# Kernel optimization log

Measured on AMD Instinct MI355X. Metric: run time of the kernel, lower is better.

The kernel has to match this reference:

```python
import jax, jax.numpy as jnp
import numpy as np

N_NODES = 50000

def gcn_conv(x, src, dst, W, b, n_nodes):
    # PyG GCNConv: add self-loops, symmetric deg^{-1/2} normalization,
    # linear transform, scatter-add aggregation (source -> target), bias.
    loop = jnp.arange(n_nodes, dtype=src.dtype)
    src2 = jnp.concatenate([src, loop])
    dst2 = jnp.concatenate([dst, loop])
    deg = jax.ops.segment_sum(jnp.ones_like(dst2, dtype=x.dtype), dst2, num_segments=n_nodes)
    dinv = jnp.where(deg > 0, jax.lax.rsqrt(deg), 0.0)
    norm = dinv[src2] * dinv[dst2]  # [E + N]
    h = x @ W                        # [N, out]
    msg = h[src2] * norm[:, None]    # gather + scale
    out = jax.ops.segment_sum(msg, dst2, num_segments=n_nodes)
    return out + b

def setup_inputs() -> dict:
    key = jax.random.key(0)
    k1, k2, k3, k4 = jax.random.split(key, 4)
    x = jax.random.normal(k1, (N_NODES, 64), dtype=jnp.float32)
    edge_index = jax.random.randint(k2, (2, 800000), 0, N_NODES, dtype=jnp.int64)
    # Glorot-ish init for weights
    W1 = jax.random.normal(k3, (64, 128), dtype=jnp.float32) * (1.0 / np.sqrt(64))
    b1 = jnp.zeros((128,), dtype=jnp.float32)
    W2 = jax.random.normal(k4, (128, 8), dtype=jnp.float32) * (1.0 / np.sqrt(128))
    b2 = jnp.zeros((8,), dtype=jnp.float32)
    return {"x": x, "edge_index": edge_index, "W1": W1, "b1": b1, "W2": W2, "b2": b2}

def reference(x, edge_index, W1, b1, W2, b2):
    src, dst = edge_index[0], edge_index[1]
    h = gcn_conv(x, src, dst, W1, b1, N_NODES)
    h = jax.nn.relu(h)
    out = gcn_conv(h, src, dst, W2, b2, N_NODES)
    return out
```

## Files before the change

kernel.cpp:

```cpp
#include <hip/hip_runtime.h>

#define IN1 64
#define MID 128
#define OUT2 8
#define YPAD 136
#define TPAD 68
#define CAP 64

__device__ __forceinline__ unsigned short f2bf(float f) {
    unsigned int u = __float_as_uint(f);
    unsigned int r = (u + 0x7fff + ((u >> 16) & 1)) >> 16;
    return (unsigned short)r;
}
__device__ __forceinline__ float bflo(unsigned int u) { return __uint_as_float(u << 16); }
__device__ __forceinline__ float bfhi(unsigned int u) { return __uint_as_float(u & 0xffff0000u); }

__global__ __launch_bounds__(256) void k_fillp(const int* __restrict__ src,
                                               const int* __restrict__ dst,
                                               int* __restrict__ cnt,
                                               unsigned short* __restrict__ col,
                                               int E4, int E, int npx, int slices) {
    int xcd = blockIdx.x & 7;
    int slice = blockIdx.x >> 3;
    int lo = xcd * npx, hi = lo + npx;
    int eps = (E4 + slices - 1) / slices;
    int g0 = slice * eps, g1 = min(E4, g0 + eps);
    int g = g0 + (int)threadIdx.x;
    if (g < g1) {
        int4 dv = ((const int4*)dst)[g];
        for (;;) {
            int gn = g + 256;
            bool has = gn < g1;
            int4 dn;
            if (has) dn = ((const int4*)dst)[gn];
            if (dv.x >= lo && dv.x < hi) {
                int p = atomicAdd(&cnt[dv.x], 1);
                if (p < CAP) col[dv.x * CAP + p] = (unsigned short)src[4 * g];
            }
            if (dv.y >= lo && dv.y < hi) {
                int p = atomicAdd(&cnt[dv.y], 1);
                if (p < CAP) col[dv.y * CAP + p] = (unsigned short)src[4 * g + 1];
            }
            if (dv.z >= lo && dv.z < hi) {
                int p = atomicAdd(&cnt[dv.z], 1);
                if (p < CAP) col[dv.z * CAP + p] = (unsigned short)src[4 * g + 2];
            }
            if (dv.w >= lo && dv.w < hi) {
                int p = atomicAdd(&cnt[dv.w], 1);
                if (p < CAP) col[dv.w * CAP + p] = (unsigned short)src[4 * g + 3];
            }
            if (!has) break;
            dv = dn;
            g = gn;
        }
    }
    if (blockIdx.x == 0 && threadIdx.x == 0) {
        for (int e = E4 * 4; e < E; ++e) {
            int d = dst[e];
            int p = atomicAdd(&cnt[d], 1);
            if (p < CAP) col[d * CAP + p] = (unsigned short)src[e];
        }
    }
}

__global__ void k_prescale(const float4* __restrict__ x4, const int* __restrict__ cnt,
                           float* __restrict__ dinv, ushort4* __restrict__ xb4, int n16) {
    int gid = blockIdx.x * blockDim.x + threadIdx.x;
    if (gid >= n16) return;
    int row = gid >> 4;
    float d = rsqrtf((float)(cnt[row] + 1));
    if ((gid & 15) == 0) dinv[row] = d;
    float4 vx = x4[gid];
    ushort4 p;
    p.x = f2bf(vx.x * d); p.y = f2bf(vx.y * d);
    p.z = f2bf(vx.z * d); p.w = f2bf(vx.w * d);
    xb4[gid] = p;
}

__global__ __launch_bounds__(256) void k_node(const uint4* __restrict__ xb4,
                                              const int* __restrict__ cnt,
                                              const unsigned short* __restrict__ col,
                                              const float* __restrict__ dinv,
                                              const float* __restrict__ W1,
                                              const float* __restrict__ b1,
                                              const float* __restrict__ W2,
                                              float* __restrict__ z, int n) {
    __shared__ float w2s[MID * OUT2];
    __shared__ float tS[4][8][TPAD];
    __shared__ float yS[4][8][YPAD];

    int t = threadIdx.x;
    ((float4*)w2s)[t] = ((const float4*)W2)[t];

    int lane = t & 63, wave = t >> 6;
    int g = lane >> 3;
    int fl = lane & 7;
    int row0 = blockIdx.x * 32 + wave * 8;
    int row = row0 + g;
    bool valid = row < n;

    float a0=0.f,a1=0.f,a2=0.f,a3=0.f,a4=0.f,a5=0.f,a6=0.f,a7=0.f;
    int deg = 0, base = 0;
    if (valid) {
        deg = min(cnt[row], CAP);
        base = row * CAP;
        uint4 u = xb4[(size_t)row * 8 + fl];
        a0 = bflo(u.x); a1 = bfhi(u.x); a2 = bflo(u.y); a3 = bfhi(u.y);
        a4 = bflo(u.z); a5 = bfhi(u.z); a6 = bflo(u.w); a7 = bfhi(u.w);
    }
    int cv = (deg >= 8) ? col[base + fl] : 0;
    int j = 0;
    for (; j + 8 <= deg; j += 8) {
        int cvn = (j + 16 <= deg) ? col[base + j + 8 + fl] : 0;
#pragma unroll
        for (int p = 0; p < 8; ++p) {
            int s = __shfl(cv, (g << 3) + p, 64);
            uint4 u = xb4[(size_t)s * 8 + fl];
            a0 += bflo(u.x); a1 += bfhi(u.x); a2 += bflo(u.y); a3 += bfhi(u.y);
            a4 += bflo(u.z); a5 += bfhi(u.z); a6 += bflo(u.w); a7 += bfhi(u.w);
        }
        cv = cvn;
    }
    int rem = deg - j;
    if (rem > 0) {
        int cvr = col[base + min(j + fl, CAP - 1)];
#pragma unroll
        for (int p = 0; p < 8; ++p) {
            if (p < rem) {
                int s = __shfl(cvr, (g << 3) + p, 64);
                uint4 u = xb4[(size_t)s * 8 + fl];
                a0 += bflo(u.x); a1 += bfhi(u.x); a2 += bflo(u.y); a3 += bfhi(u.y);
                a4 += bflo(u.z); a5 += bfhi(u.z); a6 += bflo(u.w); a7 += bfhi(u.w);
            }
        }
    }
    {
        float4 w0 = {a0, a1, a2, a3};
        float4 w1v = {a4, a5, a6, a7};
        *(float4*)&tS[wave][g][8 * fl] = w0;
        *(float4*)&tS[wave][g][8 * fl + 4] = w1v;
    }

    float dnd[8];
#pragma unroll
    for (int k = 0; k < 8; ++k) dnd[k] = dinv[min(row0 + k, n - 1)];

    float ya[8], yb[8];
#pragma unroll
    for (int i = 0; i < 8; ++i) { ya[i] = 0.f; yb[i] = 0.f; }
#pragma unroll 2
    for (int k4 = 0; k4 < IN1; k4 += 4) {
        float4 tv[8];
#pragma unroll
        for (int nd = 0; nd < 8; ++nd) tv[nd] = *(const float4*)&tS[wave][nd][k4];
#pragma unroll
        for (int kk = 0; kk < 4; ++kk) {
            int k = k4 + kk;
            float wa = W1[k * MID + lane];
            float wb = W1[k * MID + lane + 64];
#pragma unroll
            for (int nd = 0; nd < 8; ++nd) {
                float e = (&tv[nd].x)[kk];
                ya[nd] = fmaf(e, wa, ya[nd]);
                yb[nd] = fmaf(e, wb, yb[nd]);
            }
        }
    }
    float bl = b1[lane], bh = b1[lane + 64];
#pragma unroll
    for (int nd = 0; nd < 8; ++nd) {
        yS[wave][nd][lane] = fmaxf(fmaf(ya[nd], dnd[nd], bl), 0.f);
        yS[wave][nd][lane + 64] = fmaxf(fmaf(yb[nd], dnd[nd], bh), 0.f);
    }

    __syncthreads();

    int nd2 = lane >> 3, ch = lane & 7;
    float p[OUT2];
#pragma unroll
    for (int c = 0; c < OUT2; ++c) p[c] = 0.0f;
#pragma unroll
    for (int kk = 0; kk < 16; ++kk) {
        int k = kk * 8 + ch;
        float yk = yS[wave][nd2][k];
        float4 wlo = *(const float4*)&w2s[k * OUT2];
        float4 whi = *(const float4*)&w2s[k * OUT2 + 4];
        p[0] = fmaf(yk, wlo.x, p[0]); p[1] = fmaf(yk, wlo.y, p[1]);
        p[2] = fmaf(yk, wlo.z, p[2]); p[3] = fmaf(yk, wlo.w, p[3]);
        p[4] = fmaf(yk, whi.x, p[4]); p[5] = fmaf(yk, whi.y, p[5]);
        p[6] = fmaf(yk, whi.z, p[6]); p[7] = fmaf(yk, whi.w, p[7]);
    }
#pragma unroll
    for (int off = 1; off < 8; off <<= 1) {
#pragma unroll
        for (int c = 0; c < OUT2; ++c) p[c] += __shfl_xor(p[c], off, 64);
    }
    int rw = row0 + nd2;
    if (rw < n) {
        z[(size_t)rw * OUT2 + ch] = p[ch] * dinv[rw];
    }
}

__global__ __launch_bounds__(256) void k_gather2(const int* __restrict__ cnt,
                                                 const unsigned short* __restrict__ col,
                                                 const float* __restrict__ z,
                                                 const float* __restrict__ dinv,
                                                 const float* __restrict__ b2,
                                                 float* __restrict__ out, int n) {
    int t = threadIdx.x, lane = t & 63, wave = t >> 6;
    int node = blockIdx.x * 4 + wave;
    if (node >= n) return;
    int nb = lane >> 3, c = lane & 7;
    float acc = (nb == 0) ? z[(size_t)node * OUT2 + c] : 0.0f;
    int deg = min(cnt[node], CAP);
    int base = node * CAP;
    int j = nb;
    if (j + 8 < deg) {
        int s0 = col[base + j], s1 = col[base + j + 8];
        for (; j + 8 < deg;) {
            int jn = j + 16;
            int t0 = 0, t1 = 0;
            bool has = jn + 8 < deg;
            if (has) { t0 = col[base + jn]; t1 = col[base + jn + 8]; }
            acc += z[(size_t)s0 * OUT2 + c] + z[(size_t)s1 * OUT2 + c];
            j = jn;
            if (!has) break;
            s0 = t0; s1 = t1;
        }
    }
    if (j < deg) acc += z[(size_t)col[base + j] * OUT2 + c];
#pragma unroll
    for (int off = 8; off < 64; off <<= 1) acc += __shfl_xor(acc, off, 64);
    if (lane < OUT2) out[(size_t)node * OUT2 + lane] = fmaf(acc, dinv[node], b2[lane]);
}

extern "C" void kernel_launch(void* const* d_in, const int* in_sizes, int n_in,
                              void* d_out, int out_size, void* d_ws, size_t ws_size,
                              hipStream_t stream) {
    const float* x  = (const float*)d_in[0];
    const int*   ei = (const int*)d_in[1];
    const float* W1 = (const float*)d_in[2];
    const float* b1 = (const float*)d_in[3];
    const float* W2 = (const float*)d_in[4];
    const float* b2 = (const float*)d_in[5];
    float* out = (float*)d_out;

    int N = in_sizes[0] / IN1;
    int E = in_sizes[1] / 2;
    const int* src = ei;
    const int* dst = ei + E;

    int* cnt = (int*)d_ws;
    unsigned short* col = (unsigned short*)(cnt + N);
    float* dinv = (float*)(col + (size_t)N * CAP);
    float* z = dinv + N;
    unsigned short* xb = (unsigned short*)(z + (size_t)N * OUT2);

    const int B = 256;
    int E4 = E / 4;
    int npx = (N + 7) / 8;
    int slices = 256;

    hipMemsetAsync(cnt, 0, (size_t)N * sizeof(int), stream);
    k_fillp<<<slices * 8, B, 0, stream>>>(src, dst, cnt, col, E4, E, npx, slices);
    k_prescale<<<((size_t)N * 16 + B - 1) / B, B, 0, stream>>>((const float4*)x, cnt, dinv,
                                                               (ushort4*)xb, N * 16);
    k_node<<<(N + 31) / 32, 256, 0, stream>>>((const uint4*)xb, cnt, col, dinv, W1, b1, W2, z, N);
    k_gather2<<<(N + 3) / 4, 256, 0, stream>>>(cnt, col, z, dinv, b2, out, N);
}
```

Before: 162.1 us.

## Fuse pipeline into two cooperative kernels with grid-wide syncs

```diff
diff --git a/kernel.cpp b/kernel.cpp
--- a/kernel.cpp
+++ b/kernel.cpp
@@ -1,4 +1,7 @@
 #include <hip/hip_runtime.h>
+#include <hip/hip_cooperative_groups.h>
+
+namespace cg = cooperative_groups;
 
 #define IN1 64
 #define MID 128
@@ -15,11 +18,14 @@
 __device__ __forceinline__ float bflo(unsigned int u) { return __uint_as_float(u << 16); }
 __device__ __forceinline__ float bfhi(unsigned int u) { return __uint_as_float(u & 0xffff0000u); }
 
-__global__ __launch_bounds__(256) void k_fillp(const int* __restrict__ src,
-                                               const int* __restrict__ dst,
-                                               int* __restrict__ cnt,
-                                               unsigned short* __restrict__ col,
-                                               int E4, int E, int npx, int slices) {
+__global__ __launch_bounds__(256, 8) void k_fill(const int* __restrict__ src,
+                                                 const int* __restrict__ dst,
+                                                 int* __restrict__ cnt,
+                                                 unsigned short* __restrict__ col,
+                                                 int E4, int E, int npx, int slices, int N) {
+    for (int i = blockIdx.x * 256 + (int)threadIdx.x; i < N; i += gridDim.x * 256) cnt[i] = 0;
+    cg::this_grid().sync();
+
     int xcd = blockIdx.x & 7;
     int slice = blockIdx.x >> 3;
     int lo = xcd * npx, hi = lo + npx;
@@ -63,175 +69,178 @@
     }
 }
 
-__global__ void k_prescale(const float4* __restrict__ x4, const int* __restrict__ cnt,
-                           float* __restrict__ dinv, ushort4* __restrict__ xb4, int n16) {
-    int gid = blockIdx.x * blockDim.x + threadIdx.x;
-    if (gid >= n16) return;
-    int row = gid >> 4;
-    float d = rsqrtf((float)(cnt[row] + 1));
-    if ((gid & 15) == 0) dinv[row] = d;
-    float4 vx = x4[gid];
-    ushort4 p;
-    p.x = f2bf(vx.x * d); p.y = f2bf(vx.y * d);
-    p.z = f2bf(vx.z * d); p.w = f2bf(vx.w * d);
-    xb4[gid] = p;
-}
-
-__global__ __launch_bounds__(256) void k_node(const uint4* __restrict__ xb4,
-                                              const int* __restrict__ cnt,
-                                              const unsigned short* __restrict__ col,
-                                              const float* __restrict__ dinv,
-                                              const float* __restrict__ W1,
-                                              const float* __restrict__ b1,
-                                              const float* __restrict__ W2,
-                                              float* __restrict__ z, int n) {
+__global__ __launch_bounds__(256, 4) void k_mlp(const float4* __restrict__ x4,
+                                                const int* __restrict__ cnt,
+                                                const unsigned short* __restrict__ col,
+                                                float* dinv,
+                                                unsigned short* xb,
+                                                const float* __restrict__ W1,
+                                                const float* __restrict__ b1,
+                                                const float* __restrict__ W2,
+                                                const float* __restrict__ b2,
+                                                float* z,
+                                                float* __restrict__ out,
+                                                int n, int n16) {
     __shared__ float w2s[MID * OUT2];
     __shared__ float tS[4][8][TPAD];
     __shared__ float yS[4][8][YPAD];
 
     int t = threadIdx.x;
+
+    for (int gid = blockIdx.x * 256 + t; gid < n16; gid += gridDim.x * 256) {
+        int row = gid >> 4;
+        float d = rsqrtf((float)(cnt[row] + 1));
+        if ((gid & 15) == 0) dinv[row] = d;
+        float4 vx = x4[gid];
+        ushort4 pv;
+        pv.x = f2bf(vx.x * d); pv.y = f2bf(vx.y * d);
+        pv.z = f2bf(vx.z * d); pv.w = f2bf(vx.w * d);
+        ((ushort4*)xb)[gid] = pv;
+    }
+    cg::this_grid().sync();
+
     ((float4*)w2s)[t] = ((const float4*)W2)[t];
+    __syncthreads();
 
     int lane = t & 63, wave = t >> 6;
     int g = lane >> 3;
     int fl = lane & 7;
-    int row0 = blockIdx.x * 32 + wave * 8;
-    int row = row0 + g;
-    bool valid = row < n;
-
-    float a0=0.f,a1=0.f,a2=0.f,a3=0.f,a4=0.f,a5=0.f,a6=0.f,a7=0.f;
-    int deg = 0, base = 0;
-    if (valid) {
-        deg = min(cnt[row], CAP);
-        base = row * CAP;
-        uint4 u = xb4[(size_t)row * 8 + fl];
-        a0 = bflo(u.x); a1 = bfhi(u.x); a2 = bflo(u.y); a3 = bfhi(u.y);
-        a4 = bflo(u.z); a5 = bfhi(u.z); a6 = bflo(u.w); a7 = bfhi(u.w);
-    }
-    int cv = (deg >= 8) ? col[base + fl] : 0;
-    int j = 0;
-    for (; j + 8 <= deg; j += 8) {
-        int cvn = (j + 16 <= deg) ? col[base + j + 8 + fl] : 0;
-#pragma unroll
-        for (int p = 0; p < 8; ++p) {
-            int s = __shfl(cv, (g << 3) + p, 64);
-            uint4 u = xb4[(size_t)s * 8 + fl];
-            a0 += bflo(u.x); a1 += bfhi(u.x); a2 += bflo(u.y); a3 += bfhi(u.y);
-            a4 += bflo(u.z); a5 += bfhi(u.z); a6 += bflo(u.w); a7 += bfhi(u.w);
-        }
-        cv = cvn;
-    }
-    int rem = deg - j;
-    if (rem > 0) {
-        int cvr = col[base + min(j + fl, CAP - 1)];
-#pragma unroll
-        for (int p = 0; p < 8; ++p) {
-            if (p < rem) {
-                int s = __shfl(cvr, (g << 3) + p, 64);
+    const uint4* xb4 = (const uint4*)xb;
+
+    int nlb = (n + 31) >> 5;
+    for (int lb = blockIdx.x; lb < nlb; lb += gridDim.x) {
+        int row0 = lb * 32 + wave * 8;
+        int row = row0 + g;
+        bool valid = row < n;
+
+        float a0=0.f,a1=0.f,a2=0.f,a3=0.f,a4=0.f,a5=0.f,a6=0.f,a7=0.f;
+        int deg = 0, base = 0;
+        if (valid) {
+            deg = min(cnt[row], CAP);
+            base = row * CAP;
+            uint4 u = xb4[(size_t)row * 8 + fl];
+            a0 = bflo(u.x); a1 = bfhi(u.x); a2 = bflo(u.y); a3 = bfhi(u.y);
+            a4 = bflo(u.z); a5 = bfhi(u.z); a6 = bflo(u.w); a7 = bfhi(u.w);
+        }
+        int cv = (deg >= 8) ? col[base + fl] : 0;
+        int j = 0;
+        for (; j + 8 <= deg; j += 8) {
+            int cvn = (j + 16 <= deg) ? col[base + j + 8 + fl] : 0;
+#pragma unroll
+            for (int p = 0; p < 8; ++p) {
+                int s = __shfl(cv, (g << 3) + p, 64);
                 uint4 u = xb4[(size_t)s * 8 + fl];
                 a0 += bflo(u.x); a1 += bfhi(u.x); a2 += bflo(u.y); a3 += bfhi(u.y);
                 a4 += bflo(u.z); a5 += bfhi(u.z); a6 += bflo(u.w); a7 += bfhi(u.w);
             }
-        }
-    }
+            cv = cvn;
+        }
+        int rem = deg - j;
+        if (rem > 0) {
+            int cvr = col[base + min(j + fl, CAP - 1)];
+#pragma unroll
+            for (int p = 0; p < 8; ++p) {
+                if (p < rem) {
+                    int s = __shfl(cvr, (g << 3) + p, 64);
+                    uint4 u = xb4[(size_t)s * 8 + fl];
+                    a0 += bflo(u.x); a1 += bfhi(u.x); a2 += bflo(u.y); a3 += bfhi(u.y);
+                    a4 += bflo(u.z); a5 += bfhi(u.z); a6 += bflo(u.w); a7 += bfhi(u.w);
+                }
+            }
+        }
+        {
+            float4 w0 = {a0, a1, a2, a3};
+            float4 w1v = {a4, a5, a6, a7};
+            *(float4*)&tS[wave][g][8 * fl] = w0;
+            *(float4*)&tS[wave][g][8 * fl + 4] = w1v;
+        }
+
+        float dnd[8];
+#pragma unroll
+        for (int k = 0; k < 8; ++k) dnd[k] = dinv[min(row0 + k, n - 1)];
+
+        float ya[8], yb[8];
+#pragma unroll
+        for (int i = 0; i < 8; ++i) { ya[i] = 0.f; yb[i] = 0.f; }
+#pragma unroll 2
+        for (int k4 = 0; k4 < IN1; k4 += 4) {
+            float4 tv[8];
+#pragma unroll
+            for (int nd = 0; nd < 8; ++nd) tv[nd] = *(const float4*)&tS[wave][nd][k4];
+#pragma unroll
+            for (int kk = 0; kk < 4; ++kk) {
+                int k = k4 + kk;
+                float wa = W1[k * MID + lane];
+                float wb = W1[k * MID + lane + 64];
+#pragma unroll
+                for (int nd = 0; nd < 8; ++nd) {
+                    float e = (&tv[nd].x)[kk];
+                    ya[nd] = fmaf(e, wa, ya[nd]);
+                    yb[nd] = fmaf(e, wb, yb[nd]);
+                }
+            }
+        }
+        float bl = b1[lane], bh = b1[lane + 64];
+#pragma unroll
+        for (int nd = 0; nd < 8; ++nd) {
+            yS[wave][nd][lane] = fmaxf(fmaf(ya[nd], dnd[nd], bl), 0.f);
+            yS[wave][nd][lane + 64] = fmaxf(fmaf(yb[nd], dnd[nd], bh), 0.f);
+        }
+
+        int nd2 = lane >> 3, ch = lane & 7;
+        float p[OUT2];
+#pragma unroll
+        for (int c = 0; c < OUT2; ++c) p[c] = 0.0f;
+#pragma unroll
+        for (int kk = 0; kk < 16; ++kk) {
+            int k = kk * 8 + ch;
+            float yk = yS[wave][nd2][k];
+            float4 wlo = *(const float4*)&w2s[k * OUT2];
+            float4 whi = *(const float4*)&w2s[k * OUT2 + 4];
+            p[0] = fmaf(yk, wlo.x, p[0]); p[1] = fmaf(yk, wlo.y, p[1]);
+            p[2] = fmaf(yk, wlo.z, p[2]); p[3] = fmaf(yk, wlo.w, p[3]);
+            p[4] = fmaf(yk, whi.x, p[4]); p[5] = fmaf(yk, whi.y, p[5]);
+            p[6] = fmaf(yk, whi.z, p[6]); p[7] = fmaf(yk, whi.w, p[7]);
+        }
+#pragma unroll
+        for (int off = 1; off < 8; off <<= 1) {
+#pragma unroll
+            for (int c = 0; c < OUT2; ++c) p[c] += __shfl_xor(p[c], off, 64);
+        }
+        int rw = row0 + nd2;
+        if (rw < n) {
+            z[(size_t)rw * OUT2 + ch] = p[ch] * dinv[rw];
+        }
+    }
+
+    cg::this_grid().sync();
+
     {
-        float4 w0 = {a0, a1, a2, a3};
-        float4 w1v = {a4, a5, a6, a7};
-        *(float4*)&tS[wave][g][8 * fl] = w0;
-        *(float4*)&tS[wave][g][8 * fl + 4] = w1v;
-    }
-
-    float dnd[8];
-#pragma unroll
-    for (int k = 0; k < 8; ++k) dnd[k] = dinv[min(row0 + k, n - 1)];
-
-    float ya[8], yb[8];
-#pragma unroll
-    for (int i = 0; i < 8; ++i) { ya[i] = 0.f; yb[i] = 0.f; }
-#pragma unroll 2
-    for (int k4 = 0; k4 < IN1; k4 += 4) {
-        float4 tv[8];
-#pragma unroll
-        for (int nd = 0; nd < 8; ++nd) tv[nd] = *(const float4*)&tS[wave][nd][k4];
-#pragma unroll
-        for (int kk = 0; kk < 4; ++kk) {
-            int k = k4 + kk;
-            float wa = W1[k * MID + lane];
-            float wb = W1[k * MID + lane + 64];
-#pragma unroll
-            for (int nd = 0; nd < 8; ++nd) {
-                float e = (&tv[nd].x)[kk];
-                ya[nd] = fmaf(e, wa, ya[nd]);
-                yb[nd] = fmaf(e, wb, yb[nd]);
-            }
-        }
-    }
-    float bl = b1[lane], bh = b1[lane + 64];
-#pragma unroll
-    for (int nd = 0; nd < 8; ++nd) {
-        yS[wave][nd][lane] = fmaxf(fmaf(ya[nd], dnd[nd], bl), 0.f);
-        yS[wave][nd][lane + 64] = fmaxf(fmaf(yb[nd], dnd[nd], bh), 0.f);
-    }
-
-    __syncthreads();
-
-    int nd2 = lane >> 3, ch = lane & 7;
-    float p[OUT2];
-#pragma unroll
-    for (int c = 0; c < OUT2; ++c) p[c] = 0.0f;
-#pragma unroll
-    for (int kk = 0; kk < 16; ++kk) {
-        int k = kk * 8 + ch;
-        float yk = yS[wave][nd2][k];
-        float4 wlo = *(const float4*)&w2s[k * OUT2];
-        float4 whi = *(const float4*)&w2s[k * OUT2 + 4];
-        p[0] = fmaf(yk, wlo.x, p[0]); p[1] = fmaf(yk, wlo.y, p[1]);
-        p[2] = fmaf(yk, wlo.z, p[2]); p[3] = fmaf(yk, wlo.w, p[3]);
-        p[4] = fmaf(yk, whi.x, p[4]); p[5] = fmaf(yk, whi.y, p[5]);
-        p[6] = fmaf(yk, whi.z, p[6]); p[7] = fmaf(yk, whi.w, p[7]);
-    }
-#pragma unroll
-    for (int off = 1; off < 8; off <<= 1) {
-#pragma unroll
-        for (int c = 0; c < OUT2; ++c) p[c] += __shfl_xor(p[c], off, 64);
-    }
-    int rw = row0 + nd2;
-    if (rw < n) {
-        z[(size_t)rw * OUT2 + ch] = p[ch] * dinv[rw];
-    }
-}
-
-__global__ __launch_bounds__(256) void k_gather2(const int* __restrict__ cnt,
-                                                 const unsigned short* __restrict__ col,
-                                                 const float* __restrict__ z,
-                                                 const float* __restrict__ dinv,
-                                                 const float* __restrict__ b2,
-                                                 float* __restrict__ out, int n) {
-    int t = threadIdx.x, lane = t & 63, wave = t >> 6;
-    int node = blockIdx.x * 4 + wave;
-    if (node >= n) return;
-    int nb = lane >> 3, c = lane & 7;
-    float acc = (nb == 0) ? z[(size_t)node * OUT2 + c] : 0.0f;
-    int deg = min(cnt[node], CAP);
-    int base = node * CAP;
-    int j = nb;
-    if (j + 8 < deg) {
-        int s0 = col[base + j], s1 = col[base + j + 8];
-        for (; j + 8 < deg;) {
-            int jn = j + 16;
-            int t0 = 0, t1 = 0;
-            bool has = jn + 8 < deg;
-            if (has) { t0 = col[base + jn]; t1 = col[base + jn + 8]; }
-            acc += z[(size_t)s0 * OUT2 + c] + z[(size_t)s1 * OUT2 + c];
-            j = jn;
-            if (!has) break;
-            s0 = t0; s1 = t1;
-        }
-    }
-    if (j < deg) acc += z[(size_t)col[base + j] * OUT2 + c];
-#pragma unroll
-    for (int off = 8; off < 64; off <<= 1) acc += __shfl_xor(acc, off, 64);
-    if (lane < OUT2) out[(size_t)node * OUT2 + lane] = fmaf(acc, dinv[node], b2[lane]);
+        int nb = lane >> 3, c = lane & 7;
+        for (int node = blockIdx.x * 4 + wave; node < n; node += gridDim.x * 4) {
+            float acc = (nb == 0) ? z[(size_t)node * OUT2 + c] : 0.0f;
+            int deg = min(cnt[node], CAP);
+            int base = node * CAP;
+            int j = nb;
+            if (j + 8 < deg) {
+                int s0 = col[base + j], s1 = col[base + j + 8];
+                for (; j + 8 < deg;) {
+                    int jn = j + 16;
+                    int t0 = 0, t1 = 0;
+                    bool has = jn + 8 < deg;
+                    if (has) { t0 = col[base + jn]; t1 = col[base + jn + 8]; }
+                    acc += z[(size_t)s0 * OUT2 + c] + z[(size_t)s1 * OUT2 + c];
+                    j = jn;
+                    if (!has) break;
+                    s0 = t0; s1 = t1;
+                }
+            }
+            if (j < deg) acc += z[(size_t)col[base + j] * OUT2 + c];
+#pragma unroll
+            for (int off = 8; off < 64; off <<= 1) acc += __shfl_xor(acc, off, 64);
+            if (lane < OUT2) out[(size_t)node * OUT2 + lane] = fmaf(acc, dinv[node], b2[lane]);
+        }
+    }
 }
 
 extern "C" void kernel_launch(void* const* d_in, const int* in_sizes, int n_in,
@@ -256,15 +265,37 @@
     float* z = dinv + N;
     unsigned short* xb = (unsigned short*)(z + (size_t)N * OUT2);
 
-    const int B = 256;
     int E4 = E / 4;
     int npx = (N + 7) / 8;
+    int n16 = N * 16;
+    const float4* x4 = (const float4*)x;
+
+    static int occ1 = 0, occ2 = 0;
+    if (occ1 == 0) {
+        int a = 0, b = 0;
+        hipError_t ea = hipOccupancyMaxActiveBlocksPerMultiprocessor(&a, (const void*)k_fill, 256, 0);
+        hipError_t eb = hipOccupancyMaxActiveBlocksPerMultiprocessor(&b, (const void*)k_mlp, 256, 0);
+        occ1 = (ea == hipSuccess && a > 0) ? a : 8;
+        occ2 = (eb == hipSuccess && b > 0) ? b : 4;
+        (void)hipGetLastError();
+    }
     int slices = 256;
-
-    hipMemsetAsync(cnt, 0, (size_t)N * sizeof(int), stream);
-    k_fillp<<<slices * 8, B, 0, stream>>>(src, dst, cnt, col, E4, E, npx, slices);
-    k_prescale<<<((size_t)N * 16 + B - 1) / B, B, 0, stream>>>((const float4*)x, cnt, dinv,
-                                                               (ushort4*)xb, N * 16);
-    k_node<<<(N + 31) / 32, 256, 0, stream>>>((const uint4*)xb, cnt, col, dinv, W1, b1, W2, z, N);
-    k_gather2<<<(N + 3) / 4, 256, 0, stream>>>(cnt, col, z, dinv, b2, out, N);
+    if (slices * 8 > occ1 * 256) slices = (occ1 * 256) / 8;
+    if (slices < 1) slices = 1;
+    int grid1 = slices * 8;
+    int grid2 = 1024;
+    if (grid2 > occ2 * 256) grid2 = occ2 * 256;
+    if (grid2 < 1) grid2 = 1;
+
+    {
+        void* args[] = {(void*)&src, (void*)&dst, (void*)&cnt, (void*)&col,
+                        (void*)&E4, (void*)&E, (void*)&npx, (void*)&slices, (void*)&N};
+        hipLaunchCooperativeKernel((const void*)k_fill, dim3(grid1), dim3(256), args, 0, stream);
+    }
+    {
+        void* args[] = {(void*)&x4, (void*)&cnt, (void*)&col, (void*)&dinv, (void*)&xb,
+                        (void*)&W1, (void*)&b1, (void*)&W2, (void*)&b2,
+                        (void*)&z, (void*)&out, (void*)&N, (void*)&n16};
+        hipLaunchCooperativeKernel((const void*)k_mlp, dim3(grid2), dim3(256), args, 0, stream);
+    }
 }
```

New measurement: 460.4 us. 2.84x slower.

## Fold prescale into fill kernel and compute degree normalization on the fly

Applied to the files above, without the earlier changes.

```diff
diff --git a/kernel.cpp b/kernel.cpp
--- a/kernel.cpp
+++ b/kernel.cpp
@@ -15,11 +15,21 @@
 __device__ __forceinline__ float bflo(unsigned int u) { return __uint_as_float(u << 16); }
 __device__ __forceinline__ float bfhi(unsigned int u) { return __uint_as_float(u & 0xffff0000u); }
 
-__global__ __launch_bounds__(256) void k_fillp(const int* __restrict__ src,
-                                               const int* __restrict__ dst,
-                                               int* __restrict__ cnt,
-                                               unsigned short* __restrict__ col,
-                                               int E4, int E, int npx, int slices) {
+__global__ __launch_bounds__(256) void k_fill(const int* __restrict__ src,
+                                              const int* __restrict__ dst,
+                                              int* __restrict__ cnt,
+                                              unsigned short* __restrict__ col,
+                                              const float4* __restrict__ x4,
+                                              ushort4* __restrict__ xb4,
+                                              int E4, int E, int npx, int slices, int n16) {
+    for (int gid = blockIdx.x * 256 + (int)threadIdx.x; gid < n16; gid += gridDim.x * 256) {
+        float4 vx = x4[gid];
+        ushort4 pv;
+        pv.x = f2bf(vx.x); pv.y = f2bf(vx.y);
+        pv.z = f2bf(vx.z); pv.w = f2bf(vx.w);
+        xb4[gid] = pv;
+    }
+
     int xcd = blockIdx.x & 7;
     int slice = blockIdx.x >> 3;
     int lo = xcd * npx, hi = lo + npx;
@@ -28,29 +38,30 @@
     int g = g0 + (int)threadIdx.x;
     if (g < g1) {
         int4 dv = ((const int4*)dst)[g];
+        int4 sv = ((const int4*)src)[g];
         for (;;) {
             int gn = g + 256;
             bool has = gn < g1;
-            int4 dn;
-            if (has) dn = ((const int4*)dst)[gn];
+            int4 dn, sn;
+            if (has) { dn = ((const int4*)dst)[gn]; sn = ((const int4*)src)[gn]; }
             if (dv.x >= lo && dv.x < hi) {
                 int p = atomicAdd(&cnt[dv.x], 1);
-                if (p < CAP) col[dv.x * CAP + p] = (unsigned short)src[4 * g];
+                if (p < CAP) col[dv.x * CAP + p] = (unsigned short)sv.x;
             }
             if (dv.y >= lo && dv.y < hi) {
                 int p = atomicAdd(&cnt[dv.y], 1);
-                if (p < CAP) col[dv.y * CAP + p] = (unsigned short)src[4 * g + 1];
+                if (p < CAP) col[dv.y * CAP + p] = (unsigned short)sv.y;
             }
             if (dv.z >= lo && dv.z < hi) {
                 int p = atomicAdd(&cnt[dv.z], 1);
-                if (p < CAP) col[dv.z * CAP + p] = (unsigned short)src[4 * g + 2];
+                if (p < CAP) col[dv.z * CAP + p] = (unsigned short)sv.z;
             }
             if (dv.w >= lo && dv.w < hi) {
                 int p = atomicAdd(&cnt[dv.w], 1);
-                if (p < CAP) col[dv.w * CAP + p] = (unsigned short)src[4 * g + 3];
+                if (p < CAP) col[dv.w * CAP + p] = (unsigned short)sv.w;
             }
             if (!has) break;
-            dv = dn;
+            dv = dn; sv = sn;
             g = gn;
         }
     }
@@ -63,24 +74,9 @@
     }
 }
 
-__global__ void k_prescale(const float4* __restrict__ x4, const int* __restrict__ cnt,
-                           float* __restrict__ dinv, ushort4* __restrict__ xb4, int n16) {
-    int gid = blockIdx.x * blockDim.x + threadIdx.x;
-    if (gid >= n16) return;
-    int row = gid >> 4;
-    float d = rsqrtf((float)(cnt[row] + 1));
-    if ((gid & 15) == 0) dinv[row] = d;
-    float4 vx = x4[gid];
-    ushort4 p;
-    p.x = f2bf(vx.x * d); p.y = f2bf(vx.y * d);
-    p.z = f2bf(vx.z * d); p.w = f2bf(vx.w * d);
-    xb4[gid] = p;
-}
-
 __global__ __launch_bounds__(256) void k_node(const uint4* __restrict__ xb4,
                                               const int* __restrict__ cnt,
                                               const unsigned short* __restrict__ col,
-                                              const float* __restrict__ dinv,
                                               const float* __restrict__ W1,
                                               const float* __restrict__ b1,
                                               const float* __restrict__ W2,
@@ -102,11 +98,15 @@
     float a0=0.f,a1=0.f,a2=0.f,a3=0.f,a4=0.f,a5=0.f,a6=0.f,a7=0.f;
     int deg = 0, base = 0;
     if (valid) {
-        deg = min(cnt[row], CAP);
+        int c0 = cnt[row];
+        deg = min(c0, CAP);
         base = row * CAP;
+        float dself = rsqrtf((float)(c0 + 1));
         uint4 u = xb4[(size_t)row * 8 + fl];
-        a0 = bflo(u.x); a1 = bfhi(u.x); a2 = bflo(u.y); a3 = bfhi(u.y);
-        a4 = bflo(u.z); a5 = bfhi(u.z); a6 = bflo(u.w); a7 = bfhi(u.w);
+        a0 = dself * bflo(u.x); a1 = dself * bfhi(u.x);
+        a2 = dself * bflo(u.y); a3 = dself * bfhi(u.y);
+        a4 = dself * bflo(u.z); a5 = dself * bfhi(u.z);
+        a6 = dself * bflo(u.w); a7 = dself * bfhi(u.w);
     }
     int cv = (deg >= 8) ? col[base + fl] : 0;
     int j = 0;
@@ -115,9 +115,13 @@
 #pragma unroll
         for (int p = 0; p < 8; ++p) {
             int s = __shfl(cv, (g << 3) + p, 64);
+            int cs = cnt[s];
             uint4 u = xb4[(size_t)s * 8 + fl];
-            a0 += bflo(u.x); a1 += bfhi(u.x); a2 += bflo(u.y); a3 += bfhi(u.y);
-            a4 += bflo(u.z); a5 += bfhi(u.z); a6 += bflo(u.w); a7 += bfhi(u.w);
+            float ds = rsqrtf((float)(cs + 1));
+            a0 = fmaf(ds, bflo(u.x), a0); a1 = fmaf(ds, bfhi(u.x), a1);
+            a2 = fmaf(ds, bflo(u.y), a2); a3 = fmaf(ds, bfhi(u.y), a3);
+            a4 = fmaf(ds, bflo(u.z), a4); a5 = fmaf(ds, bfhi(u.z), a5);
+            a6 = fmaf(ds, bflo(u.w), a6); a7 = fmaf(ds, bfhi(u.w), a7);
         }
         cv = cvn;
     }
@@ -128,9 +132,13 @@
         for (int p = 0; p < 8; ++p) {
             if (p < rem) {
                 int s = __shfl(cvr, (g << 3) + p, 64);
+                int cs = cnt[s];
                 uint4 u = xb4[(size_t)s * 8 + fl];
-                a0 += bflo(u.x); a1 += bfhi(u.x); a2 += bflo(u.y); a3 += bfhi(u.y);
-                a4 += bflo(u.z); a5 += bfhi(u.z); a6 += bflo(u.w); a7 += bfhi(u.w);
+                float ds = rsqrtf((float)(cs + 1));
+                a0 = fmaf(ds, bflo(u.x), a0); a1 = fmaf(ds, bfhi(u.x), a1);
+                a2 = fmaf(ds, bflo(u.y), a2); a3 = fmaf(ds, bfhi(u.y), a3);
+                a4 = fmaf(ds, bflo(u.z), a4); a5 = fmaf(ds, bfhi(u.z), a5);
+                a6 = fmaf(ds, bflo(u.w), a6); a7 = fmaf(ds, bfhi(u.w), a7);
             }
         }
     }
@@ -143,7 +151,10 @@
 
     float dnd[8];
 #pragma unroll
-    for (int k = 0; k < 8; ++k) dnd[k] = dinv[min(row0 + k, n - 1)];
+    for (int k = 0; k < 8; ++k) {
+        int ck = cnt[min(row0 + k, n - 1)];
+        dnd[k] = rsqrtf((float)(ck + 1));
+    }
 
     float ya[8], yb[8];
 #pragma unroll
@@ -197,14 +208,13 @@
     }
     int rw = row0 + nd2;
     if (rw < n) {
-        z[(size_t)rw * OUT2 + ch] = p[ch] * dinv[rw];
+        z[(size_t)rw * OUT2 + ch] = p[ch] * dnd[nd2];
     }
 }
 
 __global__ __launch_bounds__(256) void k_gather2(const int* __restrict__ cnt,
                                                  const unsigned short* __restrict__ col,
                                                  const float* __restrict__ z,
-                                                 const float* __restrict__ dinv,
                                                  const float* __restrict__ b2,
                                                  float* __restrict__ out, int n) {
     int t = threadIdx.x, lane = t & 63, wave = t >> 6;
@@ -212,7 +222,8 @@
     if (node >= n) return;
     int nb = lane >> 3, c = lane & 7;
     float acc = (nb == 0) ? z[(size_t)node * OUT2 + c] : 0.0f;
-    int deg = min(cnt[node], CAP);
+    int c0 = cnt[node];
+    int deg = min(c0, CAP);
     int base = node * CAP;
     int j = nb;
     if (j + 8 < deg) {
@@ -231,7 +242,7 @@
     if (j < deg) acc += z[(size_t)col[base + j] * OUT2 + c];
 #pragma unroll
     for (int off = 8; off < 64; off <<= 1) acc += __shfl_xor(acc, off, 64);
-    if (lane < OUT2) out[(size_t)node * OUT2 + lane] = fmaf(acc, dinv[node], b2[lane]);
+    if (lane < OUT2) out[(size_t)node * OUT2 + lane] = fmaf(acc, rsqrtf((float)(c0 + 1)), b2[lane]);
 }
 
 extern "C" void kernel_launch(void* const* d_in, const int* in_sizes, int n_in,
@@ -252,19 +263,19 @@
 
     int* cnt = (int*)d_ws;
     unsigned short* col = (unsigned short*)(cnt + N);
-    float* dinv = (float*)(col + (size_t)N * CAP);
-    float* z = dinv + N;
+    float* z = (float*)(col + (size_t)N * CAP);
     unsigned short* xb = (unsigned short*)(z + (size_t)N * OUT2);
 
     const int B = 256;
     int E4 = E / 4;
     int npx = (N + 7) / 8;
     int slices = 256;
+    int n16 = N * 16;
 
     hipMemsetAsync(cnt, 0, (size_t)N * sizeof(int), stream);
-    k_fillp<<<slices * 8, B, 0, stream>>>(src, dst, cnt, col, E4, E, npx, slices);
-    k_prescale<<<((size_t)N * 16 + B - 1) / B, B, 0, stream>>>((const float4*)x, cnt, dinv,
-                                                               (ushort4*)xb, N * 16);
-    k_node<<<(N + 31) / 32, 256, 0, stream>>>((const uint4*)xb, cnt, col, dinv, W1, b1, W2, z, N);
-    k_gather2<<<(N + 3) / 4, 256, 0, stream>>>(cnt, col, z, dinv, b2, out, N);
-}
+    k_fill<<<slices * 8, B, 0, stream>>>(src, dst, cnt, col,
+                                         (const float4*)x, (ushort4*)xb,
+                                         E4, E, npx, slices, n16);
+    k_node<<<(N + 31) / 32, 256, 0, stream>>>((const uint4*)xb, cnt, col, W1, b1, W2, z, N);
+    k_gather2<<<(N + 3) / 4, 256, 0, stream>>>(cnt, col, z, b2, out, N);
+}
```

After: 165.9 us. +2.3%, slower.
